# Kernel tuning notes

Measured on AMD Instinct MI355X. Metric: run time of the kernel, lower is better.

Reference implementation:

```python
import jax, jax.numpy as jnp
import numpy as np

NTYPE = 4
NWAVE = 8
NORBIT = 128
NIPSIN = 3
CUTOFF = 5.0
NEIGH = 64
NB = 32
NATOM = 256
NPAIR_PER = NATOM * NEIGH  # pairs per molecule

# index_para: [0, 1,1,1, 2,...x9] -> length 1 + 3 + 9 = 13
INDEX_PARA = np.concatenate([np.zeros(1, np.int32)] + [np.full(3 ** i, i, np.int32) for i in range(1, NIPSIN)])
NPARA = INDEX_PARA.shape[0]  # 13


def setup_inputs() -> dict:
    key = jax.random.key(0)
    ks = jax.random.split(key, 12)
    cart = jax.random.normal(ks[0], (NB, NATOM, 3), dtype=jnp.float32)
    numatoms = jnp.full((NB,), NATOM, dtype=jnp.int32)
    species = jax.random.randint(ks[1], (NB * NATOM,), 0, NTYPE, dtype=jnp.int32)
    atom_index = jax.random.randint(ks[2], (2, NB, NPAIR_PER), 0, NATOM, dtype=jnp.int32)
    # small nonzero shifts so no pair has exactly zero distance
    shifts = 0.1 * jax.random.normal(ks[3], (NB, NPAIR_PER, 3), dtype=jnp.float32)
    rs = jax.random.uniform(ks[4], (NTYPE, NWAVE), dtype=jnp.float32) * CUTOFF
    inta = -jnp.abs(jax.random.normal(ks[5], (NTYPE, NWAVE), dtype=jnp.float32))
    params = jnp.ones((NTYPE, NWAVE), dtype=jnp.float32) / float(NEIGH)
    hyper = 0.1 * jax.random.normal(ks[6], (NIPSIN, NWAVE, NORBIT), dtype=jnp.float32)
    oc_w0 = 0.05 * jax.random.normal(ks[7], (NORBIT, NWAVE), dtype=jnp.float32)
    oc_e0 = 0.05 * jax.random.normal(ks[8], (NTYPE, NWAVE), dtype=jnp.float32)
    oc_w1 = 0.05 * jax.random.normal(ks[9], (NORBIT, NWAVE), dtype=jnp.float32)
    oc_e1 = 0.05 * jax.random.normal(ks[10], (NTYPE, NWAVE), dtype=jnp.float32)
    return {"cart": cart, "shifts": shifts, "rs": rs, "inta": inta, "params": params,
            "hyper": hyper, "oc_w0": oc_w0, "oc_e0": oc_e0, "oc_w1": oc_w1, "oc_e1": oc_e1,
            "numatoms": numatoms, "species": species, "atom_index": atom_index}


def _angular(dist_vec, f_cut):
    # dist_vec: (N, 3), f_cut: (N,) -> (NPARA, N)
    dv = dist_vec.T  # (3, N)
    ang = f_cut[None, :]  # (1, N)
    parts = [ang]
    for _ in range(1, NIPSIN):
        ang = (ang[:, None, :] * dv[None, :, :]).reshape(-1, ang.shape[-1])
        parts.append(ang)
    return jnp.concatenate(parts, axis=0)  # (13, N)


def reference(cart, shifts, rs, inta, params, hyper, oc_w0, oc_e0, oc_w1, oc_e1,
              numatoms, species, atom_index):
    nbatch, numatom, _ = cart.shape
    totnatom = nbatch * numatom
    # global pair indices: per-molecule neighbor indices + molecule offset
    offsets = jnp.arange(nbatch, dtype=atom_index.dtype) * numatom  # (nbatch,)
    idx12 = (atom_index + offsets[None, :, None]).reshape(2, -1)  # (2, Npair)
    cart_ = cart.reshape(-1, 3)  # (totnatom, 3)
    dist_vec = cart_[idx12[0]] - cart_[idx12[1]] + shifts.reshape(-1, 3)  # (Npair, 3)
    distances = jnp.linalg.norm(dist_vec, axis=-1)  # (Npair,)
    f_cut = jnp.square(0.5 * jnp.cos(distances * (jnp.pi / CUTOFF)) + 0.5)
    sp_pair = species[idx12[1]]  # (Npair,)
    # radial gaussian: exp(inta * (d - rs)^2), per-pair type gather
    radial = jnp.exp(inta[sp_pair] * jnp.square(distances[:, None] - rs[sp_pair]))  # (Npair, nwave)
    ang = _angular(dist_vec, f_cut)  # (NPARA, Npair)
    # orbital[i, j, k] = ang[j, i] * radial[i, k]
    orbital = ang.T[:, :, None] * radial[:, None, :]  # (Npair, NPARA, nwave)
    hyper_exp = hyper[jnp.asarray(INDEX_PARA)]  # (NPARA, nwave, norbit)

    def obtain(orb_coeff):
        worbital = orbital * orb_coeff[idx12[1]][:, None, :]  # gather + scale
        sum_worbital = jax.ops.segment_sum(worbital, idx12[0], num_segments=totnatom)
        hyper_worbital = jnp.einsum('ijk,jkm->ijm', sum_worbital, hyper_exp)
        return jnp.sum(jnp.square(hyper_worbital), axis=1)  # (totnatom, norbit)

    orb_coeff = params[species]  # (totnatom, nwave)
    density = obtain(orb_coeff)
    for w, e in ((oc_w0, oc_e0), (oc_w1, oc_e1)):
        orb_coeff = orb_coeff + jnp.tanh(density @ w + e[species])
        density = obtain(orb_coeff)
    return density
```

## Files before the change

kernel.cpp:

```cpp
#include <hip/hip_runtime.h>
#include <hip/hip_bf16.h>
#include <math.h>

#define NTYPE   4
#define NWAVE   8
#define NORBIT  128
#define NEIGH   64
#define NB      32
#define NATOM   256
#define NPP     (NATOM * NEIGH)
#define NPAIR   (NB * NPP)
#define TOTATOM (NB * NATOM)
#define NPARA   13

__device__ __forceinline__ float fast_tanh(float x) {
    float ax = fabsf(x);
    float e  = __expf(-2.0f * ax);
    float r  = (1.0f - e) / (1.0f + e);
    return copysignf(r, x);
}

__global__ __launch_bounds__(1024) void k_sort(const int* __restrict__ atom_index,
                                               const float* __restrict__ cart,
                                               const float* __restrict__ shifts,
                                               const int* __restrict__ species,
                                               const float* __restrict__ params,
                                               float* __restrict__ coeff0,
                                               float4* __restrict__ rec,
                                               int* __restrict__ offs) {
    const int b = blockIdx.x;
    const int t = threadIdx.x;
    __shared__ int hist[NATOM];
    __shared__ int scan[NATOM];
    __shared__ int cur[NATOM];

    if (t < NATOM) {
        hist[t] = 0;
        int a = b * NATOM + t;
        int sp = species[a];
#pragma unroll
        for (int w = 0; w < NWAVE; w++) coeff0[a * NWAVE + w] = params[sp * NWAVE + w];
    }
    __syncthreads();

    int iloc[16];
#pragma unroll
    for (int k = 0; k < 16; k++) {
        int p = t + k * 1024;
        iloc[k] = atom_index[b * NPP + p];
        atomicAdd(&hist[iloc[k]], 1);
    }
    __syncthreads();

    if (t < NATOM) scan[t] = hist[t];
    __syncthreads();
    for (int d = 1; d < NATOM; d <<= 1) {
        int v = (t < NATOM && t >= d) ? scan[t - d] : 0;
        __syncthreads();
        if (t < NATOM) scan[t] += v;
        __syncthreads();
    }
    if (t < NATOM) {
        int ex = scan[t] - hist[t];
        cur[t] = ex;
        offs[b * NATOM + t] = b * NPP + ex;
    }
    if (b == NB - 1 && t == 0) offs[TOTATOM] = NPAIR;
    __syncthreads();

#pragma unroll
    for (int k = 0; k < 16; k++) {
        int p = t + k * 1024;
        int i = iloc[k];
        int jloc = atom_index[NPAIR + b * NPP + p];
        int ig = b * NATOM + i;
        int jg = b * NATOM + jloc;
        float dx = cart[ig * 3 + 0] - cart[jg * 3 + 0] + shifts[(b * NPP + p) * 3 + 0];
        float dy = cart[ig * 3 + 1] - cart[jg * 3 + 1] + shifts[(b * NPP + p) * 3 + 1];
        float dz = cart[ig * 3 + 2] - cart[jg * 3 + 2] + shifts[(b * NPP + p) * 3 + 2];
        int sp = species[jg];
        int pos = atomicAdd(&cur[i], 1);
        rec[b * NPP + pos] = make_float4(dx, dy, dz, __int_as_float(jg | (sp << 16)));
    }
}

__global__ __launch_bounds__(256) void k_density(const float4* __restrict__ rec,
                                                 const int* __restrict__ offs,
                                                 const float* __restrict__ coeff_in,
                                                 const float* __restrict__ rs,
                                                 const float* __restrict__ inta,
                                                 const float* __restrict__ hyper,
                                                 const float* __restrict__ W,
                                                 const float* __restrict__ E,
                                                 const int* __restrict__ species,
                                                 float* __restrict__ coeff_out,
                                                 float* __restrict__ density_out,
                                                 int mode) {
    const int wv = threadIdx.x >> 6;
    const int lane = threadIdx.x & 63;
    const int a = blockIdx.x * 4 + wv;
    const int pl = lane >> 3;
    const int w  = lane & 7;

    float rs0 = rs[0 * NWAVE + w], rs1 = rs[1 * NWAVE + w],
          rs2 = rs[2 * NWAVE + w], rs3 = rs[3 * NWAVE + w];
    float in0 = inta[0 * NWAVE + w], in1 = inta[1 * NWAVE + w],
          in2 = inta[2 * NWAVE + w], in3 = inta[3 * NWAVE + w];

    const int start = offs[a];
    const int end   = offs[a + 1];

    float S[NPARA];
#pragma unroll
    for (int k = 0; k < NPARA; k++) S[k] = 0.0f;

#pragma unroll 2
    for (int idx = start + pl; idx < end; idx += 8) {
        float4 r = rec[idx];
        int jp = __float_as_int(r.w);
        int j  = jp & 0xFFFF;
        int sp = jp >> 16;
        float cj = coeff_in[j * NWAVE + w];
        float d2 = r.x * r.x + r.y * r.y + r.z * r.z;
        float d  = sqrtf(d2);
        float c  = __cosf(d * 0.62831853071795864769f);
        float fc = 0.5f * c + 0.5f;
        fc = fc * fc;
        float rw = (sp == 0) ? rs0 : (sp == 1) ? rs1 : (sp == 2) ? rs2 : rs3;
        float iw = (sp == 0) ? in0 : (sp == 1) ? in1 : (sp == 2) ? in2 : in3;
        float dr  = d - rw;
        float rad = __expf(iw * dr * dr);
        float q = fc * rad * cj;
        S[0] += q;
        float qx = q * r.x, qy = q * r.y, qz = q * r.z;
        S[1] += qx; S[2] += qy; S[3] += qz;
        S[4]  += qx * r.x; S[5]  += qx * r.y; S[6]  += qx * r.z;
        S[7]  += qy * r.x; S[8]  += qy * r.y; S[9]  += qy * r.z;
        S[10] += qz * r.x; S[11] += qz * r.y; S[12] += qz * r.z;
    }

#pragma unroll
    for (int k = 0; k < NPARA; k++) {
        S[k] += __shfl_xor(S[k], 8, 64);
        S[k] += __shfl_xor(S[k], 16, 64);
        S[k] += __shfl_xor(S[k], 32, 64);
    }

    __shared__ float lds_S[4][NPARA * NWAVE];
    if (pl == 0) {
#pragma unroll
        for (int k = 0; k < NPARA; k++) lds_S[wv][k * NWAVE + w] = S[k];
    }
    __syncthreads();

    float acc0 = 0.0f, acc1 = 0.0f;
    const int o0 = lane, o1 = lane + 64;
#pragma unroll
    for (int para = 0; para < NPARA; para++) {
        int ip = (para == 0) ? 0 : ((para < 4) ? 1 : 2);
        const float* Hb = hyper + ip * NWAVE * NORBIT;
        float h0 = 0.0f, h1 = 0.0f;
#pragma unroll
        for (int w2 = 0; w2 < NWAVE; w2++) {
            float s = lds_S[wv][para * NWAVE + w2];
            h0 += s * Hb[w2 * NORBIT + o0];
            h1 += s * Hb[w2 * NORBIT + o1];
        }
        acc0 += h0 * h0;
        acc1 += h1 * h1;
    }

    if (mode == 1) {
        density_out[a * NORBIT + o0] = acc0;
        density_out[a * NORBIT + o1] = acc1;
        return;
    }

    float part[NWAVE];
#pragma unroll
    for (int w2 = 0; w2 < NWAVE; w2++)
        part[w2] = acc0 * W[o0 * NWAVE + w2] + acc1 * W[o1 * NWAVE + w2];
#pragma unroll
    for (int mask = 1; mask < 64; mask <<= 1) {
#pragma unroll
        for (int w2 = 0; w2 < NWAVE; w2++)
            part[w2] += __shfl_xor(part[w2], mask, 64);
    }
    if (lane < NWAVE) {
        int sp = species[a];
        coeff_out[a * NWAVE + lane] =
            coeff_in[a * NWAVE + lane] + fast_tanh(part[lane] + E[sp * NWAVE + lane]);
    }
}

extern "C" void kernel_launch(void* const* d_in, const int* in_sizes, int n_in,
                              void* d_out, int out_size, void* d_ws, size_t ws_size,
                              hipStream_t stream) {
    const float* cart    = (const float*)d_in[0];
    const float* shifts  = (const float*)d_in[1];
    const float* rs      = (const float*)d_in[2];
    const float* inta    = (const float*)d_in[3];
    const float* params  = (const float*)d_in[4];
    const float* hyper   = (const float*)d_in[5];
    const float* w0      = (const float*)d_in[6];
    const float* e0      = (const float*)d_in[7];
    const float* w1      = (const float*)d_in[8];
    const float* e1      = (const float*)d_in[9];
    const int* species    = (const int*)d_in[11];
    const int* atom_index = (const int*)d_in[12];
    float* out = (float*)d_out;

    char* ws = (char*)d_ws;
    float4* rec   = (float4*)ws;  ws += (size_t)NPAIR * 16;
    float* coeffA = (float*)ws;   ws += (size_t)TOTATOM * NWAVE * 4;
    float* coeffB = (float*)ws;   ws += (size_t)TOTATOM * NWAVE * 4;
    int* offs     = (int*)ws;     ws += (TOTATOM + 1) * 4;

    k_sort<<<NB, 1024, 0, stream>>>(atom_index, cart, shifts, species, params,
                                    coeffA, rec, offs);

    k_density<<<TOTATOM / 4, 256, 0, stream>>>(rec, offs, coeffA, rs, inta, hyper,
                                               w0, e0, species, coeffB, out, 0);
    k_density<<<TOTATOM / 4, 256, 0, stream>>>(rec, offs, coeffB, rs, inta, hyper,
                                               w1, e1, species, coeffA, out, 0);
    k_density<<<TOTATOM / 4, 256, 0, stream>>>(rec, offs, coeffA, rs, inta, hyper,
                                               w1, e1, species, coeffB, out, 1);
}
```

Before: 170.7 us.

## Split per-molecule sort into parallel histogram, offset, and scatter kernels

The single 32-block counting-sort kernel is replaced by three kernels: per-chunk histograms across 256 blocks, a per-molecule scan that produces per-chunk start offsets, and a 256-block scatter that reads positions and species from LDS. This spreads the sort across many more CUs, where before only 32 blocks ran. The density kernel also gains software prefetch of the next pair record and a reorganised hyper contraction that reads the per-wave sums as float4 from a padded LDS layout. The cost is two extra launches and extra workspace traffic for the partial histograms.

```diff
diff --git a/kernel.cpp b/kernel.cpp
--- a/kernel.cpp
+++ b/kernel.cpp
@@ -13,6 +13,10 @@
 #define TOTATOM (NB * NATOM)
 #define NPARA   13
 
+#define CHUNK   2048
+#define BPB     8
+#define NBLK    (NB * BPB)
+
 __device__ __forceinline__ float fast_tanh(float x) {
     float ax = fabsf(x);
     float e  = __expf(-2.0f * ax);
@@ -20,67 +24,90 @@
     return copysignf(r, x);
 }
 
-__global__ __launch_bounds__(1024) void k_sort(const int* __restrict__ atom_index,
-                                               const float* __restrict__ cart,
-                                               const float* __restrict__ shifts,
-                                               const int* __restrict__ species,
-                                               const float* __restrict__ params,
-                                               float* __restrict__ coeff0,
-                                               float4* __restrict__ rec,
-                                               int* __restrict__ offs) {
-    const int b = blockIdx.x;
-    const int t = threadIdx.x;
+__global__ __launch_bounds__(256) void k_hist(const int* __restrict__ atom_index,
+                                              int* __restrict__ histpart) {
+    const int bl = blockIdx.x, t = threadIdx.x;
+    const int b = bl >> 3, c = bl & 7;
     __shared__ int hist[NATOM];
+    hist[t] = 0;
+    __syncthreads();
+    const int base = b * NPP + c * CHUNK;
+#pragma unroll
+    for (int k = 0; k < CHUNK / 256; k++) {
+        int i = atom_index[base + t + k * 256];
+        atomicAdd(&hist[i], 1);
+    }
+    __syncthreads();
+    histpart[bl * NATOM + t] = hist[t];
+}
+
+__global__ __launch_bounds__(256) void k_offsets(const int* __restrict__ histpart,
+                                                 int* __restrict__ startpart,
+                                                 int* __restrict__ offs,
+                                                 const int* __restrict__ species,
+                                                 const float* __restrict__ params,
+                                                 float* __restrict__ coeff0) {
+    const int b = blockIdx.x, t = threadIdx.x;
+    int h[BPB];
+    int tot = 0;
+#pragma unroll
+    for (int c = 0; c < BPB; c++) {
+        h[c] = histpart[(b * BPB + c) * NATOM + t];
+        tot += h[c];
+    }
     __shared__ int scan[NATOM];
+    scan[t] = tot;
+    __syncthreads();
+    for (int d = 1; d < NATOM; d <<= 1) {
+        int v = (t >= d) ? scan[t - d] : 0;
+        __syncthreads();
+        scan[t] += v;
+        __syncthreads();
+    }
+    int run = b * NPP + (scan[t] - tot);
+    offs[b * NATOM + t] = run;
+    if (b == 0 && t == 0) offs[TOTATOM] = NPAIR;
+#pragma unroll
+    for (int c = 0; c < BPB; c++) {
+        startpart[(b * BPB + c) * NATOM + t] = run;
+        run += h[c];
+    }
+    int a = b * NATOM + t;
+    int sp = species[a];
+#pragma unroll
+    for (int w = 0; w < NWAVE; w++) coeff0[a * NWAVE + w] = params[sp * NWAVE + w];
+}
+
+__global__ __launch_bounds__(256) void k_scatter(const int* __restrict__ atom_index,
+                                                 const float* __restrict__ cart,
+                                                 const float* __restrict__ shifts,
+                                                 const int* __restrict__ species,
+                                                 const int* __restrict__ startpart,
+                                                 float4* __restrict__ rec) {
+    const int bl = blockIdx.x, t = threadIdx.x;
+    const int b = bl >> 3, c = bl & 7;
     __shared__ int cur[NATOM];
-
-    if (t < NATOM) {
-        hist[t] = 0;
-        int a = b * NATOM + t;
-        int sp = species[a];
-#pragma unroll
-        for (int w = 0; w < NWAVE; w++) coeff0[a * NWAVE + w] = params[sp * NWAVE + w];
-    }
-    __syncthreads();
-
-    int iloc[16];
-#pragma unroll
-    for (int k = 0; k < 16; k++) {
-        int p = t + k * 1024;
-        iloc[k] = atom_index[b * NPP + p];
-        atomicAdd(&hist[iloc[k]], 1);
-    }
-    __syncthreads();
-
-    if (t < NATOM) scan[t] = hist[t];
-    __syncthreads();
-    for (int d = 1; d < NATOM; d <<= 1) {
-        int v = (t < NATOM && t >= d) ? scan[t - d] : 0;
-        __syncthreads();
-        if (t < NATOM) scan[t] += v;
-        __syncthreads();
-    }
-    if (t < NATOM) {
-        int ex = scan[t] - hist[t];
-        cur[t] = ex;
-        offs[b * NATOM + t] = b * NPP + ex;
-    }
-    if (b == NB - 1 && t == 0) offs[TOTATOM] = NPAIR;
-    __syncthreads();
-
-#pragma unroll
-    for (int k = 0; k < 16; k++) {
-        int p = t + k * 1024;
-        int i = iloc[k];
-        int jloc = atom_index[NPAIR + b * NPP + p];
-        int ig = b * NATOM + i;
-        int jg = b * NATOM + jloc;
-        float dx = cart[ig * 3 + 0] - cart[jg * 3 + 0] + shifts[(b * NPP + p) * 3 + 0];
-        float dy = cart[ig * 3 + 1] - cart[jg * 3 + 1] + shifts[(b * NPP + p) * 3 + 1];
-        float dz = cart[ig * 3 + 2] - cart[jg * 3 + 2] + shifts[(b * NPP + p) * 3 + 2];
-        int sp = species[jg];
+    __shared__ float cx[NATOM], cy[NATOM], cz[NATOM];
+    __shared__ int spl[NATOM];
+    cur[t] = startpart[bl * NATOM + t];
+    const int ag = b * NATOM + t;
+    cx[t] = cart[ag * 3 + 0];
+    cy[t] = cart[ag * 3 + 1];
+    cz[t] = cart[ag * 3 + 2];
+    spl[t] = species[ag];
+    __syncthreads();
+    const int base = b * NPP + c * CHUNK;
+#pragma unroll
+    for (int k = 0; k < CHUNK / 256; k++) {
+        int p = base + t + k * 256;
+        int i = atom_index[p];
+        int j = atom_index[NPAIR + p];
+        float dx = cx[i] - cx[j] + shifts[p * 3 + 0];
+        float dy = cy[i] - cy[j] + shifts[p * 3 + 1];
+        float dz = cz[i] - cz[j] + shifts[p * 3 + 2];
+        int jg = b * NATOM + j;
         int pos = atomicAdd(&cur[i], 1);
-        rec[b * NPP + pos] = make_float4(dx, dy, dz, __int_as_float(jg | (sp << 16)));
+        rec[pos] = make_float4(dx, dy, dz, __int_as_float(jg | (spl[j] << 16)));
     }
 }
 
@@ -102,10 +129,8 @@
     const int pl = lane >> 3;
     const int w  = lane & 7;
 
-    float rs0 = rs[0 * NWAVE + w], rs1 = rs[1 * NWAVE + w],
-          rs2 = rs[2 * NWAVE + w], rs3 = rs[3 * NWAVE + w];
-    float in0 = inta[0 * NWAVE + w], in1 = inta[1 * NWAVE + w],
-          in2 = inta[2 * NWAVE + w], in3 = inta[3 * NWAVE + w];
+    float rs0 = rs[w],      rs1 = rs[8 + w],  rs2 = rs[16 + w], rs3 = rs[24 + w];
+    float in0 = inta[w],    in1 = inta[8 + w], in2 = inta[16 + w], in3 = inta[24 + w];
 
     const int start = offs[a];
     const int end   = offs[a + 1];
@@ -114,9 +139,13 @@
 #pragma unroll
     for (int k = 0; k < NPARA; k++) S[k] = 0.0f;
 
-#pragma unroll 2
-    for (int idx = start + pl; idx < end; idx += 8) {
-        float4 r = rec[idx];
+    int idx = start + pl;
+    float4 r = make_float4(0.f, 0.f, 0.f, 0.f);
+    if (idx < end) r = rec[idx];
+    for (; idx < end; idx += 8) {
+        int nidx = idx + 8;
+        float4 rn = r;
+        if (nidx < end) rn = rec[nidx];
         int jp = __float_as_int(r.w);
         int j  = jp & 0xFFFF;
         int sp = jp >> 16;
@@ -137,6 +166,7 @@
         S[4]  += qx * r.x; S[5]  += qx * r.y; S[6]  += qx * r.z;
         S[7]  += qy * r.x; S[8]  += qy * r.y; S[9]  += qy * r.z;
         S[10] += qz * r.x; S[11] += qz * r.y; S[12] += qz * r.z;
+        r = rn;
     }
 
 #pragma unroll
@@ -146,28 +176,49 @@
         S[k] += __shfl_xor(S[k], 32, 64);
     }
 
-    __shared__ float lds_S[4][NPARA * NWAVE];
+    __shared__ float lds_S[4][NWAVE * 16];
     if (pl == 0) {
 #pragma unroll
-        for (int k = 0; k < NPARA; k++) lds_S[wv][k * NWAVE + w] = S[k];
-    }
-    __syncthreads();
-
+        for (int k = 0; k < NPARA; k++) lds_S[wv][w * 16 + k] = S[k];
+    }
+    __syncthreads();
+
+    const int o0 = lane, o1 = lane + 64;
+    float hw0[NPARA], hw1[NPARA];
+#pragma unroll
+    for (int k = 0; k < NPARA; k++) { hw0[k] = 0.0f; hw1[k] = 0.0f; }
+#pragma unroll
+    for (int w2 = 0; w2 < NWAVE; w2++) {
+        const float* Sw = &lds_S[wv][w2 * 16];
+        float4 s0 = *(const float4*)(Sw);
+        float4 s1 = *(const float4*)(Sw + 4);
+        float4 s2 = *(const float4*)(Sw + 8);
+        float  sc = Sw[12];
+        float h00 = hyper[w2 * NORBIT + o0];
+        float h01 = hyper[w2 * NORBIT + o1];
+        float h10 = hyper[(NWAVE + w2) * NORBIT + o0];
+        float h11 = hyper[(NWAVE + w2) * NORBIT + o1];
+        float h20 = hyper[(2 * NWAVE + w2) * NORBIT + o0];
+        float h21 = hyper[(2 * NWAVE + w2) * NORBIT + o1];
+        hw0[0]  += s0.x * h00; hw1[0]  += s0.x * h01;
+        hw0[1]  += s0.y * h10; hw1[1]  += s0.y * h11;
+        hw0[2]  += s0.z * h10; hw1[2]  += s0.z * h11;
+        hw0[3]  += s0.w * h10; hw1[3]  += s0.w * h11;
+        hw0[4]  += s1.x * h20; hw1[4]  += s1.x * h21;
+        hw0[5]  += s1.y * h20; hw1[5]  += s1.y * h21;
+        hw0[6]  += s1.z * h20; hw1[6]  += s1.z * h21;
+        hw0[7]  += s1.w * h20; hw1[7]  += s1.w * h21;
+        hw0[8]  += s2.x * h20; hw1[8]  += s2.x * h21;
+        hw0[9]  += s2.y * h20; hw1[9]  += s2.y * h21;
+        hw0[10] += s2.z * h20; hw1[10] += s2.z * h21;
+        hw0[11] += s2.w * h20; hw1[11] += s2.w * h21;
+        hw0[12] += sc   * h20; hw1[12] += sc   * h21;
+    }
     float acc0 = 0.0f, acc1 = 0.0f;
-    const int o0 = lane, o1 = lane + 64;
-#pragma unroll
-    for (int para = 0; para < NPARA; para++) {
-        int ip = (para == 0) ? 0 : ((para < 4) ? 1 : 2);
-        const float* Hb = hyper + ip * NWAVE * NORBIT;
-        float h0 = 0.0f, h1 = 0.0f;
-#pragma unroll
-        for (int w2 = 0; w2 < NWAVE; w2++) {
-            float s = lds_S[wv][para * NWAVE + w2];
-            h0 += s * Hb[w2 * NORBIT + o0];
-            h1 += s * Hb[w2 * NORBIT + o1];
-        }
-        acc0 += h0 * h0;
-        acc1 += h1 * h1;
+#pragma unroll
+    for (int k = 0; k < NPARA; k++) {
+        acc0 += hw0[k] * hw0[k];
+        acc1 += hw1[k] * hw1[k];
     }
 
     if (mode == 1) {
@@ -211,13 +262,17 @@
     float* out = (float*)d_out;
 
     char* ws = (char*)d_ws;
-    float4* rec   = (float4*)ws;  ws += (size_t)NPAIR * 16;
-    float* coeffA = (float*)ws;   ws += (size_t)TOTATOM * NWAVE * 4;
-    float* coeffB = (float*)ws;   ws += (size_t)TOTATOM * NWAVE * 4;
-    int* offs     = (int*)ws;     ws += (TOTATOM + 1) * 4;
-
-    k_sort<<<NB, 1024, 0, stream>>>(atom_index, cart, shifts, species, params,
-                                    coeffA, rec, offs);
+    float4* rec    = (float4*)ws;  ws += (size_t)NPAIR * 16;
+    float* coeffA  = (float*)ws;   ws += (size_t)TOTATOM * NWAVE * 4;
+    float* coeffB  = (float*)ws;   ws += (size_t)TOTATOM * NWAVE * 4;
+    int* offs      = (int*)ws;     ws += (TOTATOM + 1) * 4;
+    ws = (char*)(((uintptr_t)ws + 255) & ~(uintptr_t)255);
+    int* histpart  = (int*)ws;     ws += (size_t)NBLK * NATOM * 4;
+    int* startpart = (int*)ws;     ws += (size_t)NBLK * NATOM * 4;
+
+    k_hist<<<NBLK, 256, 0, stream>>>(atom_index, histpart);
+    k_offsets<<<NB, 256, 0, stream>>>(histpart, startpart, offs, species, params, coeffA);
+    k_scatter<<<NBLK, 256, 0, stream>>>(atom_index, cart, shifts, species, startpart, rec);
 
     k_density<<<TOTATOM / 4, 256, 0, stream>>>(rec, offs, coeffA, rs, inta, hyper,
                                                w0, e0, species, coeffB, out, 0);
```

New measurement: 148.9 us. 1.15x faster.
